# Kernel tuning notes

Measured on AMD Instinct MI355X. Metric: run time of the kernel, lower is better.

## Reference

```python
import jax, jax.numpy as jnp
import numpy as np

B, T, D, H = 4, 2048, 1024, 16
HD = D // H  # 64
NEG = -np.finfo(np.float32).max


def setup_inputs() -> dict:
    key = jax.random.key(0)
    ks = jax.random.split(key, 9)
    s = 1.0 / np.sqrt(D)
    return {
        "x": jax.random.normal(ks[0], (B, T, D), jnp.float32),
        "wq": jax.random.normal(ks[1], (D, D), jnp.float32) * s,
        "bq": jax.random.normal(ks[2], (D,), jnp.float32) * 0.02,
        "wk": jax.random.normal(ks[3], (D, D), jnp.float32) * s,
        "bk": jax.random.normal(ks[4], (D,), jnp.float32) * 0.02,
        "wv": jax.random.normal(ks[5], (D, D), jnp.float32) * s,
        "bv": jax.random.normal(ks[6], (D,), jnp.float32) * 0.02,
        "wo": jax.random.normal(ks[7], (D, D), jnp.float32) * s,
        "bo": jax.random.normal(ks[8], (D,), jnp.float32) * 0.02,
    }


def reference(x, wq, bq, wk, bk, wv, bv, wo, bo):
    b, t, d = x.shape
    # separate Q, K, V projections, reshape to (B, H, T, HD)
    def proj(w, bias):
        y = x @ w + bias
        return y.reshape(b, t, H, HD).transpose(0, 2, 1, 3)
    q = proj(wq, bq)
    k = proj(wk, bk)
    v = proj(wv, bv)
    scale = 1.0 / np.sqrt(HD).astype(np.float32)
    scores = jnp.einsum("bhqd,bhkd->bhqk", q, k) * scale  # (B,H,T,T)
    # causal mask: -max_float on strictly upper triangle (matches source)
    mask = jnp.triu(jnp.full((t, t), NEG, jnp.float32), k=1)
    attn = jax.nn.softmax(scores + mask, axis=-1)
    out = jnp.einsum("bhqk,bhkd->bhqd", attn, v)
    out = out.transpose(0, 2, 1, 3).reshape(b, t, d)
    return out @ wo + bo
```

## Files before the change

### kernel.cpp

```cpp
#include <hip/hip_runtime.h>

typedef __bf16 bf16x8 __attribute__((ext_vector_type(8)));
typedef float f32x4 __attribute__((ext_vector_type(4)));

#define B_ 4
#define T_ 2048
#define D_ 1024
#define H_ 16
#define HD_ 64
#define M_ 8192
#define QSCALE 0.1803368801111204f

__device__ __forceinline__ ushort f2b(float f) {
  union { float f; unsigned u; } v; v.f = f;
  unsigned u = v.u;
  return (ushort)((u + 0x7FFFu + ((u >> 16) & 1u)) >> 16);
}

__device__ __forceinline__ unsigned pkbf(float a, float b) {
  union { float f; unsigned u; } va, vb; va.f = a; vb.f = b;
  return __builtin_amdgcn_perm(vb.u + 0x8000u, va.u + 0x8000u, 0x07060302u);
}

__device__ __forceinline__ void gll16(const void* g, void* l) {
  __builtin_amdgcn_global_load_lds(
      (const __attribute__((address_space(1))) unsigned*)g,
      (__attribute__((address_space(3))) unsigned*)l, 16, 0, 0);
}

__global__ __launch_bounds__(256) void prep_kernel(
    const float* __restrict__ x,
    const float* __restrict__ wq, const float* __restrict__ wk,
    const float* __restrict__ wv, const float* __restrict__ wo,
    ushort* __restrict__ xb, ushort* __restrict__ wt_qkv,
    ushort* __restrict__ wt_o) {
  __shared__ float tile[32][33];
  int bid = blockIdx.x;
  if (bid < 8192) {
    int idx = bid * 256 + threadIdx.x;
    float4 v = ((const float4*)x)[idx];
    ushort4 o;
    o.x = f2b(v.x); o.y = f2b(v.y); o.z = f2b(v.z); o.w = f2b(v.w);
    ((ushort4*)xb)[idx] = o;
  } else {
    int i2 = bid - 8192;
    int z = i2 >> 10;
    int rem = i2 & 1023;
    const float* src = (z == 0) ? wq : (z == 1) ? wk : (z == 2) ? wv : wo;
    ushort* dst = (z < 3) ? (wt_qkv + (size_t)z * D_ * D_) : wt_o;
    int n0 = (rem & 31) * 32, k0 = (rem >> 5) * 32;
    int tx = threadIdx.x & 31, ty = threadIdx.x >> 5;
    for (int i = 0; i < 4; i++) {
      int r = ty + i * 8;
      tile[r][tx] = src[(size_t)(k0 + r) * D_ + n0 + tx];
    }
    __syncthreads();
    for (int i = 0; i < 4; i++) {
      int r = ty + i * 8;
      dst[(size_t)(n0 + r) * D_ + k0 + tx] = f2b(tile[tx][r]);
    }
  }
}

__global__ __launch_bounds__(512) void gemm_pipe_kernel(
    const ushort* __restrict__ A, const ushort* __restrict__ Bt,
    const float* __restrict__ bias_q, const float* __restrict__ bias_k,
    const float* __restrict__ bias_v,
    ushort* __restrict__ qb, ushort* __restrict__ kb, ushort* __restrict__ vtb) {
  extern __shared__ char lds_raw[];
  ushort (*As)[256][64] = (ushort (*)[256][64])lds_raw;
  ushort (*Bs)[128][64] = (ushort (*)[128][64])(lds_raw + 98304);
  int tid = threadIdx.x;
  int wave = tid >> 6, lane = tid & 63, lrow = lane >> 4, lcol = lane & 15;
  int wr = wave >> 1, wc = wave & 1;

  int gx = gridDim.x;
  int nwg = gx * gridDim.y;
  int orig = blockIdx.x + gx * blockIdx.y;
  int work = (orig & 7) * (nwg >> 3) + (orig >> 3);
  int m0 = (work / gx) * 256, n0 = (work % gx) * 128;

  int r_s = tid >> 3, c_s = tid & 7;
  int scv = c_s ^ (r_s & 7);
  const ushort* aB = A + (size_t)(m0 + r_s) * D_ + scv * 8;
  const ushort* bB = Bt + (size_t)(n0 + r_s) * D_ + scv * 8;

  auto stageA = [&](int buf, int t, int u) {
    const ushort* s = aB + (size_t)u * 128 * D_ + t * 64;
    char* d = (char*)&As[buf][0][0] + u * 16384 + tid * 16;
    gll16(s, d);
    gll16(s + (size_t)64 * D_, d + 8192);
  };
  auto stageB = [&](int buf, int t) {
    const ushort* s = bB + t * 64;
    char* d = (char*)&Bs[buf][0][0] + tid * 16;
    gll16(s, d);
    gll16(s + (size_t)64 * D_, d + 8192);
  };

  f32x4 zero = {0.f, 0.f, 0.f, 0.f};
  f32x4 acc[4][4];
  for (int i = 0; i < 4; i++)
    for (int j = 0; j < 4; j++) acc[i][j] = zero;

  int swz = lcol & 7;

  stageA(0, 0, 0); stageA(0, 0, 1); stageB(0, 0);
  stageA(1, 1, 0); stageA(1, 1, 1); stageB(1, 1);
  asm volatile("s_waitcnt vmcnt(6)" ::: "memory");
  __builtin_amdgcn_sched_barrier(0);
  __builtin_amdgcn_s_barrier();

#pragma unroll
  for (int t = 0; t < 16; ++t) {
    int buf = t % 3;
    int nb = (t + 2) % 3;
#pragma unroll
    for (int ks = 0; ks < 2; ++ks) {
      bf16x8 af[4], bf[4];
      int ch = ((ks * 4 + lrow) ^ swz) * 8;
#pragma unroll
      for (int mt = 0; mt < 4; mt++)
        af[mt] = *(const bf16x8*)&As[buf][wr * 64 + mt * 16 + lcol][ch];
#pragma unroll
      for (int nt = 0; nt < 4; nt++)
        bf[nt] = *(const bf16x8*)&Bs[buf][wc * 64 + nt * 16 + lcol][ch];
      if (t + 2 < 16) {
        if (ks == 0) { stageA(nb, t + 2, 0); stageA(nb, t + 2, 1); }
        else         { stageB(nb, t + 2); }
      }
      __builtin_amdgcn_sched_barrier(0);
      __builtin_amdgcn_s_barrier();
      __builtin_amdgcn_sched_barrier(0);
      __builtin_amdgcn_s_setprio(1);
#pragma unroll
      for (int mt = 0; mt < 4; mt++)
#pragma unroll
        for (int nt = 0; nt < 4; nt++)
          acc[mt][nt] = __builtin_amdgcn_mfma_f32_16x16x32_bf16(
              af[mt], bf[nt], acc[mt][nt], 0, 0, 0);
      __builtin_amdgcn_s_setprio(0);
      if (ks == 1) {
        if (t <= 13) {
          asm volatile("s_waitcnt vmcnt(6)" ::: "memory");
        } else if (t == 14) {
          asm volatile("s_waitcnt vmcnt(0)" ::: "memory");
        }
      }
      __builtin_amdgcn_sched_barrier(0);
      __builtin_amdgcn_s_barrier();
    }
  }

  {
    int proj = n0 >> 10;
    const float* bias = (proj == 0) ? bias_q : (proj == 1) ? bias_k : bias_v;
    for (int mt = 0; mt < 4; mt++) {
      int gm0 = m0 + wr * 64 + mt * 16 + lrow * 4;
      int b = gm0 >> 11, tp = gm0 & 2047;
      for (int nt = 0; nt < 4; nt++) {
        int gn = n0 + wc * 64 + nt * 16 + lcol;
        int inner = gn & 1023;
        int h = inner >> 6, hd = inner & 63;
        float bv = bias[inner];
        if (proj == 0) {
          size_t base = ((size_t)(b * H_ + h) * T_ + tp) * HD_ + hd;
          for (int r = 0; r < 4; r++)
            qb[base + (size_t)r * HD_] = f2b((acc[mt][nt][r] + bv) * QSCALE);
        } else if (proj == 1) {
          size_t base = ((size_t)(b * H_ + h) * T_ + tp) * HD_ + hd;
          for (int r = 0; r < 4; r++)
            kb[base + (size_t)r * HD_] = f2b(acc[mt][nt][r] + bv);
        } else {
          ushort4 pk;
          pk.x = f2b(acc[mt][nt][0] + bv);
          pk.y = f2b(acc[mt][nt][1] + bv);
          pk.z = f2b(acc[mt][nt][2] + bv);
          pk.w = f2b(acc[mt][nt][3] + bv);
          *(ushort4*)&vtb[((size_t)(b * H_ + h) * HD_ + hd) * T_ + tp] = pk;
        }
      }
    }
  }
}

__global__ __launch_bounds__(256) void gemm_o_kernel(
    const ushort* __restrict__ A, const ushort* __restrict__ Bt,
    const float* __restrict__ bias, float* __restrict__ outf) {
  __shared__ ushort As[2][128][64];
  __shared__ ushort Bs[2][128][64];
  int tid = threadIdx.x;
  int wave = tid >> 6, lane = tid & 63, lrow = lane >> 4, lcol = lane & 15;

  int gx = gridDim.x;
  int nwg = gx * gridDim.y;
  int orig = blockIdx.x + gx * blockIdx.y;
  int work = (orig & 7) * (nwg >> 3) + (orig >> 3);
  int m0 = (work / gx) * 128, n0 = (work % gx) * 128;
  int wm = (wave & 1) * 64, wn = (wave >> 1) * 64;

  int rb = tid >> 3;
  int dc = tid & 7;
  int scv = dc ^ (rb & 7);
  const ushort* aBase = A + (size_t)(m0 + rb) * D_ + scv * 8;
  const ushort* bBase = Bt + (size_t)(n0 + rb) * D_ + scv * 8;

  f32x4 zero = {0.f, 0.f, 0.f, 0.f};
  f32x4 acc[4][4];
  for (int i = 0; i < 4; i++)
    for (int j = 0; j < 4; j++) acc[i][j] = zero;

  int swz = lcol & 7;

  auto stage = [&](int buf, int k) {
#pragma unroll
    for (int g = 0; g < 4; g++) {
      gll16(aBase + (size_t)(32 * g) * D_ + k, &As[buf][0][0] + tid * 8 + g * 2048);
      gll16(bBase + (size_t)(32 * g) * D_ + k, &Bs[buf][0][0] + tid * 8 + g * 2048);
    }
  };

  stage(0, 0);

  for (int k0 = 0; k0 < D_; k0 += 64) {
    int cur = (k0 >> 6) & 1, nxt = cur ^ 1;
    __syncthreads();
    if (k0 + 64 < D_) stage(nxt, k0 + 64);

    for (int ks = 0; ks < 2; ks++) {
      bf16x8 af[4], bf[4];
      int ch = ((ks * 4 + lrow) ^ swz) * 8;
      for (int mt = 0; mt < 4; mt++)
        af[mt] = *(const bf16x8*)&As[cur][wm + mt * 16 + lcol][ch];
      for (int nt = 0; nt < 4; nt++)
        bf[nt] = *(const bf16x8*)&Bs[cur][wn + nt * 16 + lcol][ch];
      for (int mt = 0; mt < 4; mt++)
        for (int nt = 0; nt < 4; nt++)
          acc[mt][nt] = __builtin_amdgcn_mfma_f32_16x16x32_bf16(
              af[mt], bf[nt], acc[mt][nt], 0, 0, 0);
    }
  }

  for (int mt = 0; mt < 4; mt++) {
    int gm0 = m0 + wm + mt * 16 + lrow * 4;
    for (int nt = 0; nt < 4; nt++) {
      int gn = n0 + wn + nt * 16 + lcol;
      float bv = bias[gn];
      for (int r = 0; r < 4; r++)
        outf[(size_t)(gm0 + r) * D_ + gn] = acc[mt][nt][r] + bv;
    }
  }
}

#define QCOMP(qblk_, q0w_, qfv, accOv, accSv)                                   \
  do {                                                                          \
    f32x4 st[2][4];                                                             \
    for (int qh = 0; qh < 2; qh++)                                              \
      for (int mt = 0; mt < 4; mt++) st[qh][mt] = zero;                         \
    __builtin_amdgcn_s_setprio(1);                                              \
    _Pragma("unroll")                                                           \
    for (int ks = 0; ks < 2; ks++)                                              \
      _Pragma("unroll")                                                         \
      for (int mt = 0; mt < 4; mt++) {                                          \
        bf16x8 kf = *(const bf16x8*)&Ks2[cur][mt * 16 + lcol]                   \
                                        [((ks * 4 + lrow) ^ rsw) * 8];          \
        st[0][mt] = __builtin_amdgcn_mfma_f32_16x16x32_bf16(kf, qfv[0][ks],     \
                                                            st[0][mt], 0, 0, 0);\
        st[1][mt] = __builtin_amdgcn_mfma_f32_16x16x32_bf16(kf, qfv[1][ks],     \
                                                            st[1][mt], 0, 0, 0);\
      }                                                                         \
    __builtin_amdgcn_s_setprio(0);                                              \
    if (j >= 2 * (qblk_)) {                                                     \
      _Pragma("unroll")                                                         \
      for (int qh = 0; qh < 2; qh++) {                                          \
        int q_g = (q0w_) + qh * 16 + lcol;                                      \
        _Pragma("unroll")                                                       \
        for (int mt = 0; mt < 4; mt++)                                          \
          for (int r = 0; r < 4; r++) {                                         \
            int kv_g = j * 64 + mt * 16 + lrow * 4 + r;                         \
            if (kv_g > q_g) st[qh][mt][r] = -1e30f;                             \
          }                                                                     \
      }                                                                         \
    }                                                                           \
    _Pragma("unroll")                                                           \
    for (int qh = 0; qh < 2; qh++)                                              \
      for (int mt = 0; mt < 4; mt++)                                            \
        for (int r = 0; r < 4; r++)                                             \
          st[qh][mt][r] = __builtin_amdgcn_exp2f(st[qh][mt][r]);                \
    _Pragma("unroll")                                                           \
    for (int qh = 0; qh < 2; qh++)                                              \
      for (int mt = 0; mt < 4; mt++) {                                          \
        uint2 pk;                                                               \
        pk.x = pkbf(st[qh][mt][0], st[qh][mt][1]);                              \
        pk.y = pkbf(st[qh][mt][2], st[qh][mt][3]);                              \
        int sl = ((2 * mt + (lrow >> 1)) ^ rsw) * 8 + (lrow & 1) * 4;           \
        *(uint2*)&Ps[wave][qh * 16 + lcol][sl] = pk;                            \
      }                                                                         \
    __builtin_amdgcn_s_setprio(1);                                              \
    _Pragma("unroll")                                                           \
    for (int ks = 0; ks < 2; ks++) {                                            \
      int ch = ((ks * 4 + lrow) ^ rsw) * 8;                                     \
      bf16x8 pf0 = *(const bf16x8*)&Ps[wave][lcol][ch];                         \
      bf16x8 pf1 = *(const bf16x8*)&Ps[wave][16 + lcol][ch];                    \
      accSv[0] = __builtin_amdgcn_mfma_f32_16x16x32_bf16(af1, pf0, accSv[0],    \
                                                         0, 0, 0);              \
      accSv[1] = __builtin_amdgcn_mfma_f32_16x16x32_bf16(af1, pf1, accSv[1],    \
                                                         0, 0, 0);              \
      _Pragma("unroll")                                                         \
      for (int mt = 0; mt < 4; mt++) {                                          \
        bf16x8 vf = *(const bf16x8*)&Vs2[cur][mt * 16 + lcol][ch];              \
        accOv[0][mt] = __builtin_amdgcn_mfma_f32_16x16x32_bf16(vf, pf0,         \
                                                    accOv[0][mt], 0, 0, 0);     \
        accOv[1][mt] = __builtin_amdgcn_mfma_f32_16x16x32_bf16(vf, pf1,         \
                                                    accOv[1][mt], 0, 0, 0);     \
      }                                                                         \
    }                                                                           \
    __builtin_amdgcn_s_setprio(0);                                              \
  } while (0)

__global__ __launch_bounds__(256) void flash_kernel(
    const ushort* __restrict__ qb, const ushort* __restrict__ kb,
    const ushort* __restrict__ vtb, ushort* __restrict__ ob) {
  __shared__ ushort Ks2[2][64][64];
  __shared__ ushort Vs2[2][64][64];
  __shared__ ushort Ps[4][32][64];
  int tid = threadIdx.x;
  int wave = tid >> 6, lane = tid & 63, lrow = lane >> 4, lcol = lane & 15;

  int bid = blockIdx.x + (blockIdx.y << 3);
  int xcd = bid & 7;
  int slot = bid >> 3;
  int phase = slot >> 5;
  int j5 = slot & 31;
  int pm = j5 & 7;
  int bh = xcd * 8 + (j5 >> 3) + phase * 4;
  int p = phase ? 7 - pm : pm;
  int qbA = 15 - p, qbB = p;
  int b = bh >> 4, h = bh & 15;
  const ushort* qp = qb + (size_t)bh * T_ * HD_;
  const ushort* kh = kb + (size_t)bh * T_ * HD_;
  const ushort* vh = vtb + (size_t)bh * HD_ * T_;

  int njA = 2 * qbA + 2, njB = 2 * qbB + 2;

  int r0 = tid >> 3, dc = tid & 7;
  int wsl = (dc ^ (r0 & 7)) * 8;
  int rsw = lcol & 7;

  uint4 kr0, kr1, vr0, vr1;
  auto gload = [&](int jt) {
    kr0 = *(const uint4*)&kh[(size_t)(jt * 64 + r0) * HD_ + dc * 8];
    kr1 = *(const uint4*)&kh[(size_t)(jt * 64 + r0 + 32) * HD_ + dc * 8];
    vr0 = *(const uint4*)&vh[(size_t)r0 * T_ + jt * 64 + dc * 8];
    vr1 = *(const uint4*)&vh[(size_t)(r0 + 32) * T_ + jt * 64 + dc * 8];
  };
  auto swrite = [&](int buf) {
    *(uint4*)&Ks2[buf][r0][wsl] = kr0;
    *(uint4*)&Ks2[buf][r0 + 32][wsl] = kr1;
    *(uint4*)&Vs2[buf][r0][wsl] = vr0;
    *(uint4*)&Vs2[buf][r0 + 32][wsl] = vr1;
  };

  bf16x8 af1;
  {
    __bf16 ov = (__bf16)((lcol == 0) ? 1.0f : 0.0f);
    for (int i2 = 0; i2 < 8; i2++) af1[i2] = ov;
  }

  f32x4 zero = {0.f, 0.f, 0.f, 0.f};

  gload(0);
  swrite(0);
  gload(1);
  __syncthreads();

  int q0wA = qbA * 128 + wave * 32, q0wB = qbB * 128 + wave * 32;
  bf16x8 qfA[2][2], qfB[2][2];
#pragma unroll
  for (int qh = 0; qh < 2; qh++)
#pragma unroll
    for (int ks = 0; ks < 2; ks++) {
      qfA[qh][ks] = *(const bf16x8*)&qp[(size_t)(q0wA + qh * 16 + lcol) * HD_ +
                                        ks * 32 + lrow * 8];
      qfB[qh][ks] = *(const bf16x8*)&qp[(size_t)(q0wB + qh * 16 + lcol) * HD_ +
                                        ks * 32 + lrow * 8];
    }

  f32x4 accOA[2][4], accOB[2][4];
  f32x4 accSA[2], accSB[2];
#pragma unroll
  for (int qh = 0; qh < 2; qh++) {
    accSA[qh] = zero; accSB[qh] = zero;
    for (int mt = 0; mt < 4; mt++) { accOA[qh][mt] = zero; accOB[qh][mt] = zero; }
  }

  for (int j = 0; j < njA; j++) {
    int cur = j & 1;
    if (j * 64 <= q0wA + 31) QCOMP(qbA, q0wA, qfA, accOA, accSA);
    if (j * 64 <= q0wB + 31) QCOMP(qbB, q0wB, qfB, accOB, accSB);
    if (j + 1 < njA) swrite(cur ^ 1);
    if (j + 2 < njA) gload(j + 2);
    __syncthreads();
  }
  (void)njB;

#pragma unroll
  for (int qh = 0; qh < 2; qh++) {
    float lsum = __shfl(accSA[qh][0], lcol);
    float linv = 1.f / lsum;
    int t = q0wA + qh * 16 + lcol;
    size_t base2 = ((size_t)b * T_ + t) * D_ + h * HD_;
#pragma unroll
    for (int mt = 0; mt < 4; mt++) {
      uint2 pk;
      pk.x = pkbf(accOA[qh][mt][0] * linv, accOA[qh][mt][1] * linv);
      pk.y = pkbf(accOA[qh][mt][2] * linv, accOA[qh][mt][3] * linv);
      *(uint2*)&ob[base2 + mt * 16 + lrow * 4] = pk;
    }
  }
#pragma unroll
  for (int qh = 0; qh < 2; qh++) {
    float lsum = __shfl(accSB[qh][0], lcol);
    float linv = 1.f / lsum;
    int t = q0wB + qh * 16 + lcol;
    size_t base2 = ((size_t)b * T_ + t) * D_ + h * HD_;
#pragma unroll
    for (int mt = 0; mt < 4; mt++) {
      uint2 pk;
      pk.x = pkbf(accOB[qh][mt][0] * linv, accOB[qh][mt][1] * linv);
      pk.y = pkbf(accOB[qh][mt][2] * linv, accOB[qh][mt][3] * linv);
      *(uint2*)&ob[base2 + mt * 16 + lrow * 4] = pk;
    }
  }
}

extern "C" void kernel_launch(void* const* d_in, const int* in_sizes, int n_in,
                              void* d_out, int out_size, void* d_ws, size_t ws_size,
                              hipStream_t stream) {
  (void)in_sizes; (void)n_in; (void)out_size; (void)ws_size;
  const float* x  = (const float*)d_in[0];
  const float* wq = (const float*)d_in[1];
  const float* bq = (const float*)d_in[2];
  const float* wk = (const float*)d_in[3];
  const float* bk = (const float*)d_in[4];
  const float* wv = (const float*)d_in[5];
  const float* bv = (const float*)d_in[6];
  const float* wo = (const float*)d_in[7];
  const float* bo = (const float*)d_in[8];
  float* out = (float*)d_out;

  char* ws = (char*)d_ws;
  ushort* xb     = (ushort*)(ws);
  ushort* wt_qkv = (ushort*)(ws + 16777216);
  ushort* wt_o   = (ushort*)(ws + 23068672);
  ushort* qb     = (ushort*)(ws + 25165824);
  ushort* kb     = (ushort*)(ws + 41943040);
  ushort* vtb    = (ushort*)(ws + 58720256);
  ushort* ob     = (ushort*)(ws + 75497472);

  hipFuncSetAttribute((const void*)gemm_pipe_kernel,
                      hipFuncAttributeMaxDynamicSharedMemorySize, 147456);

  prep_kernel<<<12288, 256, 0, stream>>>(x, wq, wk, wv, wo, xb, wt_qkv, wt_o);
  gemm_pipe_kernel<<<dim3(24, 32), 512, 147456, stream>>>(xb, wt_qkv, bq, bk, bv,
                                                          qb, kb, vtb);
  flash_kernel<<<dim3(8, 64), 256, 0, stream>>>(qb, kb, vtb, ob);
  gemm_o_kernel<<<dim3(8, 64), 256, 0, stream>>>(ob, wt_o, bo, out);
}
```

Baseline: 256.3 us.

## Load K fragments directly from global into registers, dropping K shared-memory staging

K tiles are no longer staged through LDS. Each wave now loads its MFMA K fragments straight from global memory into registers, prefetching the next tile into a second register set. This removes the K LDS writes and reads and shrinks shared memory use. In exchange, all four waves redundantly fetch the same K tile from global/L2, and the extra 16 bf16x8 registers per thread raise register pressure.

Result: slower. 287.2 us (+12.1%).

```diff
diff --git a/kernel.cpp b/kernel.cpp
--- a/kernel.cpp
+++ b/kernel.cpp
@@ -252,7 +252,7 @@
   }
 }
 
-#define QCOMP(qblk_, q0w_, qfv, accOv, accSv)                                   \
+#define QCOMP(qblk_, q0w_, qfv, kfv, accOv, accSv)                              \
   do {                                                                          \
     f32x4 st[2][4];                                                             \
     for (int qh = 0; qh < 2; qh++)                                              \
@@ -262,12 +262,10 @@
     for (int ks = 0; ks < 2; ks++)                                              \
       _Pragma("unroll")                                                         \
       for (int mt = 0; mt < 4; mt++) {                                          \
-        bf16x8 kf = *(const bf16x8*)&Ks2[cur][mt * 16 + lcol]                   \
-                                        [((ks * 4 + lrow) ^ rsw) * 8];          \
-        st[0][mt] = __builtin_amdgcn_mfma_f32_16x16x32_bf16(kf, qfv[0][ks],     \
-                                                            st[0][mt], 0, 0, 0);\
-        st[1][mt] = __builtin_amdgcn_mfma_f32_16x16x32_bf16(kf, qfv[1][ks],     \
-                                                            st[1][mt], 0, 0, 0);\
+        st[0][mt] = __builtin_amdgcn_mfma_f32_16x16x32_bf16(kfv[ks * 4 + mt],   \
+                                            qfv[0][ks], st[0][mt], 0, 0, 0);    \
+        st[1][mt] = __builtin_amdgcn_mfma_f32_16x16x32_bf16(kfv[ks * 4 + mt],   \
+                                            qfv[1][ks], st[1][mt], 0, 0, 0);    \
       }                                                                         \
     __builtin_amdgcn_s_setprio(0);                                              \
     if (j >= 2 * (qblk_)) {                                                     \
@@ -321,7 +319,6 @@
 __global__ __launch_bounds__(256) void flash_kernel(
     const ushort* __restrict__ qb, const ushort* __restrict__ kb,
     const ushort* __restrict__ vtb, ushort* __restrict__ ob) {
-  __shared__ ushort Ks2[2][64][64];
   __shared__ ushort Vs2[2][64][64];
   __shared__ ushort Ps[4][32][64];
   int tid = threadIdx.x;
@@ -341,24 +338,31 @@
   const ushort* kh = kb + (size_t)bh * T_ * HD_;
   const ushort* vh = vtb + (size_t)bh * HD_ * T_;
 
-  int njA = 2 * qbA + 2, njB = 2 * qbB + 2;
+  int njA = 2 * qbA + 2;
 
   int r0 = tid >> 3, dc = tid & 7;
   int wsl = (dc ^ (r0 & 7)) * 8;
   int rsw = lcol & 7;
 
-  uint4 kr0, kr1, vr0, vr1;
-  auto gload = [&](int jt) {
-    kr0 = *(const uint4*)&kh[(size_t)(jt * 64 + r0) * HD_ + dc * 8];
-    kr1 = *(const uint4*)&kh[(size_t)(jt * 64 + r0 + 32) * HD_ + dc * 8];
+  uint4 vr0, vr1;
+  auto gloadV = [&](int jt) {
     vr0 = *(const uint4*)&vh[(size_t)r0 * T_ + jt * 64 + dc * 8];
     vr1 = *(const uint4*)&vh[(size_t)(r0 + 32) * T_ + jt * 64 + dc * 8];
   };
-  auto swrite = [&](int buf) {
-    *(uint4*)&Ks2[buf][r0][wsl] = kr0;
-    *(uint4*)&Ks2[buf][r0 + 32][wsl] = kr1;
+  auto swriteV = [&](int buf) {
     *(uint4*)&Vs2[buf][r0][wsl] = vr0;
     *(uint4*)&Vs2[buf][r0 + 32][wsl] = vr1;
+  };
+
+  bf16x8 kfc[8], kfn[8];
+  auto kfload = [&](int jt, bf16x8* kf) {
+    const ushort* kb2 = kh + (size_t)(jt * 64) * HD_;
+#pragma unroll
+    for (int ks = 0; ks < 2; ks++)
+#pragma unroll
+      for (int mt = 0; mt < 4; mt++)
+        kf[ks * 4 + mt] = *(const bf16x8*)&kb2[(size_t)(mt * 16 + lcol) * HD_ +
+                                               ks * 32 + lrow * 8];
   };
 
   bf16x8 af1;
@@ -369,9 +373,10 @@
 
   f32x4 zero = {0.f, 0.f, 0.f, 0.f};
 
-  gload(0);
-  swrite(0);
-  gload(1);
+  kfload(0, kfc);
+  gloadV(0);
+  swriteV(0);
+  gloadV(1);
   __syncthreads();
 
   int q0wA = qbA * 128 + wave * 32, q0wB = qbB * 128 + wave * 32;
@@ -396,13 +401,17 @@
 
   for (int j = 0; j < njA; j++) {
     int cur = j & 1;
-    if (j * 64 <= q0wA + 31) QCOMP(qbA, q0wA, qfA, accOA, accSA);
-    if (j * 64 <= q0wB + 31) QCOMP(qbB, q0wB, qfB, accOB, accSB);
-    if (j + 1 < njA) swrite(cur ^ 1);
-    if (j + 2 < njA) gload(j + 2);
+    if (j + 1 < njA) kfload(j + 1, kfn);
+    if (j * 64 <= q0wA + 31) QCOMP(qbA, q0wA, qfA, kfc, accOA, accSA);
+    if (j * 64 <= q0wB + 31) QCOMP(qbB, q0wB, qfB, kfc, accOB, accSB);
+    if (j + 1 < njA) swriteV(cur ^ 1);
+    if (j + 2 < njA) gloadV(j + 2);
     __syncthreads();
-  }
-  (void)njB;
+    if (j + 1 < njA) {
+#pragma unroll
+      for (int q2 = 0; q2 < 8; q2++) kfc[q2] = kfn[q2];
+    }
+  }
 
 #pragma unroll
   for (int qh = 0; qh < 2; qh++) {
```
